# Kernel optimization log

Measured on AMD Instinct MI355X. Metric: run time of the kernel, lower is better.

## Reference

```python
import jax, jax.numpy as jnp
import numpy as np

N = 262144          # number of points
L = 16              # levels per encoder
F = 2               # features per level
HMAP = 1 << 19      # hashmap entries per hashed level
BASE = 32           # base grid resolution
GROWTH = 2.0        # per-level scale
OUT_DIM = L * F * 4 # 128

# Global geographic normalization ranges (GeoAdaptiveRange.global_range())
LAT = (-90.0, 90.0)
LON = (-180.0, 180.0)
ELEV = (-11000.0, 9000.0)
TIME = (0.0, 1.0)


def _layout():
    offs, ress, hashed = [], [], []
    off = 0
    for l in range(L):
        res = int(np.ceil(BASE * GROWTH ** l))
        n = res ** 3
        size = min(n, HMAP)
        size = (size + 7) // 8 * 8  # align to 8 like tcnn/gridencoder
        offs.append(off); ress.append(res); hashed.append(n > HMAP)
        off += size
    return (np.asarray(offs, np.int32), np.asarray(ress, np.int32),
            np.asarray(hashed, np.bool_), off)

OFFSETS, RESOLUTIONS, HASHED, TABLE_SIZE = _layout()

_CORNERS = np.asarray([[(i >> 0) & 1, (i >> 1) & 1, (i >> 2) & 1] for i in range(8)], np.int32)  # [8,3]
_P0, _P1, _P2 = np.uint32(1), np.uint32(2654435761), np.uint32(805459861)  # NGP spatial-hash primes


def _encode_level(u, res, offset, use_hash, table):
    # u: [N,3] in [0,1]; res/offset/use_hash: per-level scalars; table: [T,F]
    pos = u * (res - 1).astype(u.dtype)
    p0 = jnp.clip(jnp.floor(pos).astype(jnp.int32), 0, res - 2)
    w = pos - p0.astype(u.dtype)                       # [N,3] trilinear fracs
    pc = p0[None, :, :] + _CORNERS[:, None, :]          # [8,N,3]
    dense = pc[..., 0] + res * (pc[..., 1] + res * pc[..., 2])  # [8,N]
    pcu = pc.astype(jnp.uint32)
    h = (pcu[..., 0] * _P0) ^ (pcu[..., 1] * _P1) ^ (pcu[..., 2] * _P2)
    hidx = (h & jnp.uint32(HMAP - 1)).astype(jnp.int32)
    idx = jnp.where(use_hash, hidx, dense) + offset     # [8,N]
    feats = table[idx]                                  # [8,N,F] gather
    cw = jnp.where(_CORNERS[:, None, :] == 1, w[None], 1.0 - w[None]).prod(-1)  # [8,N]
    return (feats * cw[..., None]).sum(0)               # [N,F]


def hash_encode(x, table, size=1.0):
    # x: [N,3] in [-size, size] -> multi-level hash-grid features [N, L*F]
    u = jnp.clip((x + size) / (2.0 * size), 0.0, 1.0)
    per_level = jax.vmap(_encode_level, in_axes=(None, 0, 0, 0, None))(
        u, jnp.asarray(RESOLUTIONS), jnp.asarray(OFFSETS), jnp.asarray(HASHED), table)  # [L,N,F]
    return per_level.transpose(1, 0, 2).reshape(x.shape[0], L * F)


def _norm(v, lo, hi):
    return jnp.clip((v - lo) / (hi - lo), 0.0, 1.0)


def setup_inputs() -> dict:
    key = jax.random.key(0)
    ks = jax.random.split(key, 9)
    lat = jax.random.uniform(ks[0], (N,), minval=-80.0, maxval=80.0)
    lon = jax.random.uniform(ks[1], (N,), minval=-170.0, maxval=170.0)
    elev = jax.random.uniform(ks[2], (N,), minval=-100.0, maxval=3000.0)
    t = jax.random.uniform(ks[3], (N,), minval=0.0, maxval=1.0)
    reference_coords = jnp.stack([lat, lon, elev, t], -1).astype(jnp.float32)
    # small relative offsets around the reference points
    d = jax.random.normal(ks[4], (N, 4), jnp.float32) * jnp.asarray([0.5, 0.5, 50.0, 0.05], jnp.float32)
    coords = reference_coords + d
    def tbl(k):
        return jax.random.uniform(k, (TABLE_SIZE, F), jnp.float32, minval=-1e-4, maxval=1e-4)
    return {
        "coords": coords,
        "reference_coords": reference_coords,
        "xyz_table": tbl(ks[5]),
        "xyt_table": tbl(ks[6]),
        "yzt_table": tbl(ks[7]),
        "xzt_table": tbl(ks[8]),
    }


def reference(coords, reference_coords, xyz_table, xyt_table, yzt_table, xzt_table):
    rel = coords - reference_coords
    x = _norm(rel[..., 0], *LAT)
    y = _norm(rel[..., 1], *LON)
    z = _norm(rel[..., 2], *ELEV)
    t = _norm(rel[..., 3], *TIME)
    nc = jnp.stack([x, y, z, t], -1)                    # [N,4] in [0,1]
    spatial = hash_encode(nc[..., :3], xyz_table)       # [N, L*F]
    t_s = (nc[..., 3:] * 2.0 - 1.0) * 0.9               # time -> [-0.9, 0.9]
    xyzt = jnp.concatenate([nc[..., :3], t_s], -1)
    xyt = jnp.concatenate([xyzt[..., :2], xyzt[..., 3:]], -1)
    yzt = xyzt[..., 1:]
    xzt = jnp.concatenate([xyzt[..., :1], xyzt[..., 2:]], -1)
    f_xyt = hash_encode(xyt, xyt_table)
    f_yzt = hash_encode(yzt, yzt_table)
    f_xzt = hash_encode(xzt, xzt_table)
    return jnp.concatenate([spatial, f_xyt, f_yzt, f_xzt], -1)  # [N, 128]
```

## Files before the change

kernel.cpp:

```cpp
#include <hip/hip_runtime.h>
#include <stdint.h>

#define HMAP_MASK ((1u << 19) - 1u)


__global__ __launch_bounds__(256) void u_precompute_kernel(
    const float4* __restrict__ coords,
    const float4* __restrict__ refc,
    float4* __restrict__ uout, int npts)
{
    #pragma clang fp contract(off)
    int p = blockIdx.x * 256 + threadIdx.x;
    if (p >= npts) return;
    float4 c = coords[p];
    float4 r = refc[p];
    float rx = c.x - r.x, ry = c.y - r.y, rz = c.z - r.z, rt = c.w - r.w;
    const float R180   = 1.0f / 180.0f;
    const float R360   = 1.0f / 360.0f;
    const float R20000 = 1.0f / 20000.0f;
    float x = fminf(fmaxf((rx + 90.0f)    * R180,   0.0f), 1.0f);
    float y = fminf(fmaxf((ry + 180.0f)   * R360,   0.0f), 1.0f);
    float z = fminf(fmaxf((rz + 11000.0f) * R20000, 0.0f), 1.0f);
    float tt = fminf(fmaxf(rt, 0.0f), 1.0f);
    float ts = (tt * 2.0f - 1.0f) * 0.9f;
    uout[p] = make_float4(x, y, z, ts);
}

__global__ __launch_bounds__(256) void gather_kernel(
    const float4* __restrict__ u,
    const float2* __restrict__ t0,
    const float2* __restrict__ t1,
    const float2* __restrict__ t2,
    const float2* __restrict__ t3,
    float2* __restrict__ stage, int npts, int chunks)
{
    #pragma clang fp contract(off)
    int bid = blockIdx.x;
    int xcd   = bid & 7;
    int j     = bid >> 3;
    int phase = j / chunks;
    int chunk = j - phase * chunks;
    int slice = phase * 8 + xcd;
    int table_id = slice >> 4;
    int level    = slice & 15;

    int point = chunk * 256 + threadIdx.x;
    if (point >= npts) return;

    float4 uu = u[point];
    float d0 = (table_id == 2) ? uu.y : uu.x;
    float d1 = (table_id <= 1) ? uu.y : uu.z;
    float d2 = (table_id == 0) ? uu.z : uu.w;
    const float2* tab = (table_id == 0) ? t0
                      : (table_id == 1) ? t1
                      : (table_id == 2) ? t2 : t3;

    float u0 = fminf(fmaxf((d0 + 1.0f) * 0.5f, 0.0f), 1.0f);
    float u1 = fminf(fmaxf((d1 + 1.0f) * 0.5f, 0.0f), 1.0f);
    float u2 = fminf(fmaxf((d2 + 1.0f) * 0.5f, 0.0f), 1.0f);

    int res = 32 << level;
    float resm1 = (float)(res - 1);
    float pos0 = u0 * resm1;
    float pos1 = u1 * resm1;
    float pos2 = u2 * resm1;
    int p0 = min(max((int)floorf(pos0), 0), res - 2);
    int p1 = min(max((int)floorf(pos1), 0), res - 2);
    int p2 = min(max((int)floorf(pos2), 0), res - 2);
    float w0 = pos0 - (float)p0;
    float w1 = pos1 - (float)p1;
    float w2 = pos2 - (float)p2;

    int off = (level >= 2) ? (294912 + ((level - 2) << 19)) : (level << 15);
    bool use_hash = (level >= 2);
    const float2* tabo = tab + off;

    float om0 = 1.0f - w0, om1 = 1.0f - w1, om2 = 1.0f - w2;
    float a0 = 0.0f, a1 = 0.0f;
    uint32_t ures = (uint32_t)res;

    #pragma unroll
    for (int ci = 0; ci < 8; ++ci) {
        int cx = ci & 1, cy = (ci >> 1) & 1, cz = (ci >> 2) & 1;
        uint32_t px = (uint32_t)(p0 + cx);
        uint32_t py = (uint32_t)(p1 + cy);
        uint32_t pz = (uint32_t)(p2 + cz);
        uint32_t idx;
        if (use_hash) {
            idx = (px ^ (py * 2654435761u) ^ (pz * 805459861u)) & HMAP_MASK;
        } else {
            idx = px + ures * (py + ures * pz);
        }
        float2 f = tabo[idx];
        float ww = (cx ? w0 : om0) * (cy ? w1 : om1) * (cz ? w2 : om2);
        a0 += f.x * ww;
        a1 += f.y * ww;
    }

    float2 val = make_float2(a0, a1);
    unsigned long long bits;
    __builtin_memcpy(&bits, &val, 8);
    __builtin_nontemporal_store(bits,
        (unsigned long long*)(stage + (size_t)slice * npts + point));
}

__global__ __launch_bounds__(256) void transpose_kernel(
    const float2* __restrict__ stage,
    float2* __restrict__ out, int npts)
{
    __shared__ float2 tile[64][65];
    int pbase = blockIdx.x * 64;
    int lane = threadIdx.x & 63;
    int row4 = threadIdx.x >> 6;

    #pragma unroll
    for (int s = 0; s < 64; s += 4) {
        int sub = s + row4;
        int p = pbase + lane;
        if (p < npts)
            tile[sub][lane] = stage[(size_t)sub * npts + p];
    }
    __syncthreads();
    #pragma unroll
    for (int p4 = 0; p4 < 64; p4 += 4) {
        int p = pbase + p4 + row4;
        if (p < npts) {
            float2 v = tile[lane][p4 + row4];
            unsigned long long bits;
            __builtin_memcpy(&bits, &v, 8);
            __builtin_nontemporal_store(bits,
                (unsigned long long*)(out + (size_t)p * 64 + lane));
        }
    }
}

__global__ __launch_bounds__(256) void energy4d_fallback(
    const float4* __restrict__ coords,
    const float4* __restrict__ refc,
    const float2* __restrict__ t0,
    const float2* __restrict__ t1,
    const float2* __restrict__ t2,
    const float2* __restrict__ t3,
    float2* __restrict__ out, int npts)
{
    #pragma clang fp contract(off)
    int t = threadIdx.x;
    int si = t & 7;
    int pi = t >> 3;
    int point = blockIdx.x * 32 + pi;
    if (point >= npts) return;
    int sub = (blockIdx.y << 3) + si;
    int table_id = sub >> 4;
    int level = sub & 15;

    float4 c = coords[point];
    float4 r = refc[point];
    float rx = c.x - r.x, ry = c.y - r.y, rz = c.z - r.z, rt = c.w - r.w;
    const float R180   = 1.0f / 180.0f;
    const float R360   = 1.0f / 360.0f;
    const float R20000 = 1.0f / 20000.0f;
    float x = fminf(fmaxf((rx + 90.0f)    * R180,   0.0f), 1.0f);
    float y = fminf(fmaxf((ry + 180.0f)   * R360,   0.0f), 1.0f);
    float z = fminf(fmaxf((rz + 11000.0f) * R20000, 0.0f), 1.0f);
    float tt = fminf(fmaxf(rt, 0.0f), 1.0f);
    float ts = (tt * 2.0f - 1.0f) * 0.9f;

    float d0 = (table_id == 2) ? y : x;
    float d1 = (table_id <= 1) ? y : z;
    float d2 = (table_id == 0) ? z : ts;
    const float2* tab = (table_id == 0) ? t0
                      : (table_id == 1) ? t1
                      : (table_id == 2) ? t2 : t3;

    float u0 = fminf(fmaxf((d0 + 1.0f) * 0.5f, 0.0f), 1.0f);
    float u1 = fminf(fmaxf((d1 + 1.0f) * 0.5f, 0.0f), 1.0f);
    float u2 = fminf(fmaxf((d2 + 1.0f) * 0.5f, 0.0f), 1.0f);

    int res = 32 << level;
    float resm1 = (float)(res - 1);
    float pos0 = u0 * resm1;
    float pos1 = u1 * resm1;
    float pos2 = u2 * resm1;
    int p0 = min(max((int)floorf(pos0), 0), res - 2);
    int p1 = min(max((int)floorf(pos1), 0), res - 2);
    int p2 = min(max((int)floorf(pos2), 0), res - 2);
    float w0 = pos0 - (float)p0;
    float w1 = pos1 - (float)p1;
    float w2 = pos2 - (float)p2;

    int off = (level >= 2) ? (294912 + ((level - 2) << 19)) : (level << 15);
    bool use_hash = (level >= 2);
    const float2* tabo = tab + off;

    float om0 = 1.0f - w0, om1 = 1.0f - w1, om2 = 1.0f - w2;
    float a0 = 0.0f, a1 = 0.0f;
    uint32_t ures = (uint32_t)res;

    #pragma unroll
    for (int ci = 0; ci < 8; ++ci) {
        int cx = ci & 1, cy = (ci >> 1) & 1, cz = (ci >> 2) & 1;
        uint32_t px = (uint32_t)(p0 + cx);
        uint32_t py = (uint32_t)(p1 + cy);
        uint32_t pz = (uint32_t)(p2 + cz);
        uint32_t idx;
        if (use_hash) {
            idx = (px ^ (py * 2654435761u) ^ (pz * 805459861u)) & HMAP_MASK;
        } else {
            idx = px + ures * (py + ures * pz);
        }
        float2 f = tabo[idx];
        float ww = (cx ? w0 : om0) * (cy ? w1 : om1) * (cz ? w2 : om2);
        a0 += f.x * ww;
        a1 += f.y * ww;
    }

    float2 val = make_float2(a0, a1);
    unsigned long long bits;
    __builtin_memcpy(&bits, &val, 8);
    __builtin_nontemporal_store(bits,
        (unsigned long long*)(out + (size_t)point * 64 + sub));
}

extern "C" void kernel_launch(void* const* d_in, const int* in_sizes, int n_in,
                              void* d_out, int out_size, void* d_ws, size_t ws_size,
                              hipStream_t stream) {
    const float4* coords = (const float4*)d_in[0];
    const float4* refc   = (const float4*)d_in[1];
    const float2* t0 = (const float2*)d_in[2];
    const float2* t1 = (const float2*)d_in[3];
    const float2* t2 = (const float2*)d_in[4];
    const float2* t3 = (const float2*)d_in[5];
    float2* out = (float2*)d_out;
    int npts = in_sizes[0] / 4;

    size_t u_bytes     = (size_t)npts * 16;
    size_t stage_bytes = (size_t)npts * 64 * 8;
    size_t needed = u_bytes + stage_bytes;

    if (d_ws != nullptr && ws_size >= needed) {
        float4* uws   = (float4*)d_ws;
        float2* stage = (float2*)((char*)d_ws + u_bytes);
        int chunks = (npts + 255) / 256;

        u_precompute_kernel<<<chunks, 256, 0, stream>>>(coords, refc, uws, npts);
        gather_kernel<<<64 * chunks, 256, 0, stream>>>(
            uws, t0, t1, t2, t3, stage, npts, chunks);
        transpose_kernel<<<(npts + 63) / 64, 256, 0, stream>>>(stage, out, npts);
    } else {
        int grid_x = (npts + 31) / 32;
        dim3 grid(grid_x, 8);
        energy4d_fallback<<<grid, 256, 0, stream>>>(coords, refc, t0, t1, t2, t3,
                                                    out, npts);
    }
}
```

Before: 738.7 us.

## Pair x-neighbor table loads, remap slice order, vectorize transpose

In the gather kernel, when the base x cell is even, the two x-adjacent corners are fetched with one 16-byte load, since their indices differ only in the lowest bit. Slices are reordered so each XCD works on a single table across levels, and outputs are remapped to the original column order. The transpose kernel now uses float4 loads and 16-byte nontemporal stores on full tiles, with a padded shared tile. This cuts the number of random gather transactions and widens memory accesses, at the cost of branch divergence between even and odd threads.

```diff
diff --git a/kernel.cpp b/kernel.cpp
--- a/kernel.cpp
+++ b/kernel.cpp
@@ -2,6 +2,8 @@
 #include <stdint.h>
 
 #define HMAP_MASK ((1u << 19) - 1u)
+
+typedef float f32x4_t __attribute__((ext_vector_type(4)));
 
 
 __global__ __launch_bounds__(256) void u_precompute_kernel(
@@ -40,9 +42,10 @@
     int j     = bid >> 3;
     int phase = j / chunks;
     int chunk = j - phase * chunks;
-    int slice = phase * 8 + xcd;
-    int table_id = slice >> 4;
-    int level    = slice & 15;
+    int s     = phase * 8 + xcd;
+    int table_id = s & 3;
+    int level    = s >> 2;
+    int sub_out  = table_id * 16 + level;
 
     int point = chunk * 256 + threadIdx.x;
     if (point >= npts) return;
@@ -78,58 +81,108 @@
     float om0 = 1.0f - w0, om1 = 1.0f - w1, om2 = 1.0f - w2;
     float a0 = 0.0f, a1 = 0.0f;
     uint32_t ures = (uint32_t)res;
-
-    #pragma unroll
-    for (int ci = 0; ci < 8; ++ci) {
-        int cx = ci & 1, cy = (ci >> 1) & 1, cz = (ci >> 2) & 1;
-        uint32_t px = (uint32_t)(p0 + cx);
-        uint32_t py = (uint32_t)(p1 + cy);
-        uint32_t pz = (uint32_t)(p2 + cz);
-        uint32_t idx;
-        if (use_hash) {
-            idx = (px ^ (py * 2654435761u) ^ (pz * 805459861u)) & HMAP_MASK;
-        } else {
-            idx = px + ures * (py + ures * pz);
-        }
-        float2 f = tabo[idx];
-        float ww = (cx ? w0 : om0) * (cy ? w1 : om1) * (cz ? w2 : om2);
-        a0 += f.x * ww;
-        a1 += f.y * ww;
+    uint32_t px0 = (uint32_t)p0;
+
+    if ((p0 & 1) == 0) {
+        #pragma unroll
+        for (int cj = 0; cj < 4; ++cj) {
+            int cy = cj & 1, cz = (cj >> 1) & 1;
+            uint32_t py = (uint32_t)(p1 + cy);
+            uint32_t pz = (uint32_t)(p2 + cz);
+            uint32_t idx0;
+            if (use_hash) {
+                idx0 = (px0 ^ (py * 2654435761u) ^ (pz * 805459861u)) & HMAP_MASK;
+            } else {
+                idx0 = px0 + ures * (py + ures * pz);
+            }
+            float4 qv = *reinterpret_cast<const float4*>(tabo + (idx0 & ~1u));
+            bool hi0 = (idx0 & 1u) != 0u;
+            float f0x = hi0 ? qv.z : qv.x, f0y = hi0 ? qv.w : qv.y;
+            float f1x = hi0 ? qv.x : qv.z, f1y = hi0 ? qv.y : qv.w;
+            float wy = cy ? w1 : om1;
+            float wz = cz ? w2 : om2;
+            float ww0 = (om0 * wy) * wz;
+            float ww1 = (w0  * wy) * wz;
+            a0 += f0x * ww0; a1 += f0y * ww0;
+            a0 += f1x * ww1; a1 += f1y * ww1;
+        }
+    } else {
+        #pragma unroll
+        for (int ci = 0; ci < 8; ++ci) {
+            int cx = ci & 1, cy = (ci >> 1) & 1, cz = (ci >> 2) & 1;
+            uint32_t px = (uint32_t)(p0 + cx);
+            uint32_t py = (uint32_t)(p1 + cy);
+            uint32_t pz = (uint32_t)(p2 + cz);
+            uint32_t idx;
+            if (use_hash) {
+                idx = (px ^ (py * 2654435761u) ^ (pz * 805459861u)) & HMAP_MASK;
+            } else {
+                idx = px + ures * (py + ures * pz);
+            }
+            float2 f = tabo[idx];
+            float ww = (cx ? w0 : om0) * (cy ? w1 : om1) * (cz ? w2 : om2);
+            a0 += f.x * ww;
+            a1 += f.y * ww;
+        }
     }
 
     float2 val = make_float2(a0, a1);
     unsigned long long bits;
     __builtin_memcpy(&bits, &val, 8);
     __builtin_nontemporal_store(bits,
-        (unsigned long long*)(stage + (size_t)slice * npts + point));
+        (unsigned long long*)(stage + (size_t)sub_out * npts + point));
 }
 
 __global__ __launch_bounds__(256) void transpose_kernel(
     const float2* __restrict__ stage,
     float2* __restrict__ out, int npts)
 {
-    __shared__ float2 tile[64][65];
+    __shared__ float2 tile[64][66];
     int pbase = blockIdx.x * 64;
-    int lane = threadIdx.x & 63;
-    int row4 = threadIdx.x >> 6;
-
-    #pragma unroll
-    for (int s = 0; s < 64; s += 4) {
-        int sub = s + row4;
-        int p = pbase + lane;
-        if (p < npts)
-            tile[sub][lane] = stage[(size_t)sub * npts + p];
-    }
-    __syncthreads();
-    #pragma unroll
-    for (int p4 = 0; p4 < 64; p4 += 4) {
-        int p = pbase + p4 + row4;
-        if (p < npts) {
-            float2 v = tile[lane][p4 + row4];
-            unsigned long long bits;
-            __builtin_memcpy(&bits, &v, 8);
-            __builtin_nontemporal_store(bits,
-                (unsigned long long*)(out + (size_t)p * 64 + lane));
+    int tid = threadIdx.x;
+
+    if (pbase + 64 <= npts) {
+        int l = tid & 31, r = tid >> 5;
+        #pragma unroll
+        for (int i = 0; i < 8; ++i) {
+            int sub = i * 8 + r;
+            float4 v = *reinterpret_cast<const float4*>(
+                stage + (size_t)sub * npts + pbase + 2 * l);
+            *reinterpret_cast<float4*>(&tile[sub][2 * l]) = v;
+        }
+        __syncthreads();
+        int p = tid >> 2, q = tid & 3;
+        float2* orow = out + (size_t)(pbase + p) * 64;
+        #pragma unroll
+        for (int i = 0; i < 8; ++i) {
+            int sub = q * 16 + 2 * i;
+            float2 e0 = tile[sub][p];
+            float2 e1 = tile[sub + 1][p];
+            f32x4_t v;
+            v[0] = e0.x; v[1] = e0.y; v[2] = e1.x; v[3] = e1.y;
+            __builtin_nontemporal_store(v, (f32x4_t*)(orow + sub));
+        }
+    } else {
+        int lane = tid & 63;
+        int row4 = tid >> 6;
+        #pragma unroll
+        for (int ss = 0; ss < 64; ss += 4) {
+            int sub = ss + row4;
+            int p = pbase + lane;
+            if (p < npts)
+                tile[sub][lane] = stage[(size_t)sub * npts + p];
+        }
+        __syncthreads();
+        #pragma unroll
+        for (int p4 = 0; p4 < 64; p4 += 4) {
+            int p = pbase + p4 + row4;
+            if (p < npts) {
+                float2 v = tile[lane][p4 + row4];
+                unsigned long long bits;
+                __builtin_memcpy(&bits, &v, 8);
+                __builtin_nontemporal_store(bits,
+                    (unsigned long long*)(out + (size_t)p * 64 + lane));
+            }
         }
     }
 }
```

New measurement: 926.0 us. 25.4% more time.
